# Optimization experiments

Hardware: AMD Instinct MI355X
Metric: run time of the kernel (lower is better)

The kernel has to match this reference:

```python
import jax, jax.numpy as jnp
import numpy as np

B, S, D, U = 8, 2048, 512, 512
L0, L1 = 128, 128  # limit_context (left, right)


def setup_inputs() -> dict:
    key = jax.random.key(0)
    ks = jax.random.split(key, 7)
    scale = 1.0 / np.sqrt(D).astype(np.float32)
    return {
        "x": jax.random.normal(ks[0], (B, S, D), dtype=jnp.float32),
        "Wq": jax.random.normal(ks[1], (D, U), dtype=jnp.float32) * scale,
        "Wk": jax.random.normal(ks[2], (D, U), dtype=jnp.float32) * scale,
        "Wv": jax.random.normal(ks[3], (D, U), dtype=jnp.float32) * scale,
        "bq": jnp.zeros((U,), dtype=jnp.float32),
        "bk": jnp.zeros((U,), dtype=jnp.float32),
        "bv": jnp.zeros((U,), dtype=jnp.float32),
    }


def reference(x, Wq, Wk, Wv, bq, bk, bv):
    # Linear projections for query / key / value (shared input x)
    q = x @ Wq + bq  # [B,S,U]
    k = x @ Wk + bk  # [B,S,U]
    v = x @ Wv + bv  # [B,S,U]

    inv_sqrt_dv = jnp.float32(1.0 / np.sqrt(U))
    scores = jnp.einsum("bqd,bkd->bqk", q, k) * inv_sqrt_dv  # [B,S,S]

    # Sliding-window mask: key j visible to query i iff i-L0 <= j <= i+L1.
    # Equivalent to the original per-step softmax over values[:, start:end].
    i = jnp.arange(S)[:, None]
    j = jnp.arange(S)[None, :]
    window = (j >= i - L0) & (j <= i + L1)  # [S,S]
    neg_inf = jnp.finfo(scores.dtype).min
    scores = jnp.where(window[None], scores, neg_inf)

    attn = jax.nn.softmax(scores, axis=-1)  # [B,S,S]
    return jnp.einsum("bqk,bkd->bqd", attn, v)  # [B,S,U]
```

## Files before the change

kernel.cpp:

```cpp
#include <hip/hip_runtime.h>

#define BATCH 8
#define S_LEN 2048
#define DDIM 512
#define UDIM 512
#define WIN_L 128
#define WIN_R 128
#define PP 296

typedef _Float16 f16;
typedef __attribute__((ext_vector_type(8))) _Float16 f16x8;
typedef __attribute__((ext_vector_type(4))) _Float16 f16x4;
typedef __attribute__((ext_vector_type(4))) float f32x4;

__device__ __forceinline__ void gload_lds16(const void* g, void* l) {
  __builtin_amdgcn_global_load_lds((const __attribute__((address_space(1))) void*)g,
                                   (__attribute__((address_space(3))) void*)l, 16, 0, 0);
}

__global__ void cast_f32_f16(const float* __restrict__ in, f16* __restrict__ out, int n) {
  int i = (blockIdx.x * blockDim.x + threadIdx.x) * 4;
  if (i < n) {
    float4 v = *(const float4*)(in + i);
    f16x4 o;
    o[0] = (f16)v.x; o[1] = (f16)v.y; o[2] = (f16)v.z; o[3] = (f16)v.w;
    *(f16x4*)(out + i) = o;
  }
}

__global__ void transpose_w(const float* __restrict__ Wq, const float* __restrict__ Wk,
                            const float* __restrict__ Wv, f16* __restrict__ WT) {
  const float* W = blockIdx.z == 0 ? Wq : (blockIdx.z == 1 ? Wk : Wv);
  f16* WTz = WT + (size_t)blockIdx.z * DDIM * UDIM;
  __shared__ float t[32][33];
  int tx = threadIdx.x & 31, ty = threadIdx.x >> 5;
  int n0 = blockIdx.x * 32, k0 = blockIdx.y * 32;
  for (int i = 0; i < 4; i++) {
    int r = ty * 4 + i;
    t[r][tx] = W[(size_t)(k0 + r) * UDIM + n0 + tx];
  }
  __syncthreads();
  for (int i = 0; i < 4; i++) {
    int r = ty * 4 + i;
    WTz[(size_t)(n0 + r) * DDIM + k0 + tx] = (f16)t[tx][r];
  }
}

__global__ __launch_bounds__(256, 2) void gemm_qkv(
    const f16* __restrict__ X, const f16* __restrict__ WT,
    const float* __restrict__ bq, const float* __restrict__ bk, const float* __restrict__ bv,
    f16* __restrict__ QKV, f16* __restrict__ VT) {
  int z = blockIdx.z;
  const f16* WTz = WT + (size_t)z * DDIM * UDIM;
  const float* bias = z == 0 ? bq : (z == 1 ? bk : bv);
  f16* out = QKV + (size_t)z * (BATCH * S_LEN) * UDIM;

  __shared__ f16 Al[2][128 * 32];
  __shared__ f16 Bl[2][128 * 32];

  int tid = threadIdx.x, wv = tid >> 6, ln = tid & 63;
  int m0 = blockIdx.x * 128, n0 = blockIdx.y * 128;
  int wm = (wv >> 1) * 64, wn = (wv & 1) * 64;
  int lm = ln & 15, lq = ln >> 4;
  int srow = ln >> 2, scol = (ln & 3) * 8;

  f32x4 acc[4][4];
  for (int mt = 0; mt < 4; mt++)
    for (int nt = 0; nt < 4; nt++)
      for (int r = 0; r < 4; r++) acc[mt][nt][r] = 0.f;

  for (int k0 = 0; k0 < DDIM; k0 += 64) {
    for (int half = 0; half < 2; half++) {
      int r0 = half * 64 + wv * 16;
      for (int c = 0; c < 2; c++) {
        gload_lds16(X + (size_t)(m0 + r0 + srow) * DDIM + k0 + c * 32 + scol, &Al[c][r0 * 32]);
        gload_lds16(WTz + (size_t)(n0 + r0 + srow) * DDIM + k0 + c * 32 + scol, &Bl[c][r0 * 32]);
      }
    }
    __syncthreads();
#pragma unroll
    for (int c = 0; c < 2; c++) {
      f16x8 af[4], bfr[4];
      for (int mt = 0; mt < 4; mt++) af[mt] = *(const f16x8*)&Al[c][(wm + mt * 16 + lm) * 32 + lq * 8];
      for (int nt = 0; nt < 4; nt++) bfr[nt] = *(const f16x8*)&Bl[c][(wn + nt * 16 + lm) * 32 + lq * 8];
      for (int mt = 0; mt < 4; mt++)
        for (int nt = 0; nt < 4; nt++)
          acc[mt][nt] = __builtin_amdgcn_mfma_f32_16x16x32_f16(af[mt], bfr[nt], acc[mt][nt], 0, 0, 0);
    }
    __syncthreads();
  }

  if (z == 2) {
    for (int mt = 0; mt < 4; mt++)
      for (int nt = 0; nt < 4; nt++) {
        int col = n0 + wn + nt * 16 + lm;
        float bv_ = bias[col];
        int row0 = m0 + wm + mt * 16 + lq * 4;
        int bb = row0 >> 11, ss = row0 & 2047;
        f16x4 o;
        for (int r = 0; r < 4; r++) o[r] = (f16)(acc[mt][nt][r] + bv_);
        *(f16x4*)&VT[((size_t)bb * UDIM + col) * S_LEN + ss] = o;
      }
  } else {
    for (int mt = 0; mt < 4; mt++)
      for (int nt = 0; nt < 4; nt++) {
        int col = n0 + wn + nt * 16 + lm;
        float bv_ = bias[col];
        for (int r = 0; r < 4; r++) {
          int row = m0 + wm + mt * 16 + lq * 4 + r;
          out[(size_t)row * UDIM + col] = (f16)(acc[mt][nt][r] + bv_);
        }
      }
  }
}

__global__ __launch_bounds__(256, 2) void attn(
    const f16* __restrict__ Q, const f16* __restrict__ K, const f16* __restrict__ VT,
    float* __restrict__ out) {
  __shared__ f16 Pb[32 * PP];
  __shared__ float wmax[2][32], wsum[2][32];

  int tid = threadIdx.x, wv = tid >> 6, ln = tid & 63;
  int lm = ln & 15, lq = ln >> 4;
  int b = blockIdx.x, q0 = blockIdx.y * 32;
  int rh = wv & 1, ch = wv >> 1;
  const size_t base = (size_t)b * S_LEN;
  const int strip0 = q0 - WIN_L;

  f16x8 qf[16];
  {
    const f16* qrow = Q + (base + q0 + rh * 16 + lm) * (size_t)DDIM + lq * 8;
#pragma unroll
    for (int kk = 0; kk < 16; kk++) qf[kk] = *(const f16x8*)(qrow + kk * 32);
  }

  f32x4 sacc[9];
#pragma unroll
  for (int t = 0; t < 9; t++)
    for (int r = 0; r < 4; r++) sacc[t][r] = 0.f;
#pragma unroll
  for (int t = 0; t < 9; t++) {
    int key = strip0 + ch * 144 + t * 16 + lm;
    int kc = key < 0 ? 0 : (key > S_LEN - 1 ? S_LEN - 1 : key);
    const f16* kp = K + (base + kc) * (size_t)DDIM + lq * 8;
#pragma unroll
    for (int kk = 0; kk < 16; kk++) {
      f16x8 bf = *(const f16x8*)(kp + kk * 32);
      sacc[t] = __builtin_amdgcn_mfma_f32_16x16x32_f16(qf[kk], bf, sacc[t], 0, 0, 0);
    }
  }

  const float scale = 0.044194173824159216f;
  float mx[4] = {-1e30f, -1e30f, -1e30f, -1e30f};
#pragma unroll
  for (int t = 0; t < 9; t++) {
    int kj = strip0 + ch * 144 + t * 16 + lm;
#pragma unroll
    for (int r = 0; r < 4; r++) {
      int qi = q0 + rh * 16 + lq * 4 + r;
      float s = sacc[t][r] * scale;
      bool ok = (kj >= 0) && (kj < S_LEN) && (kj >= qi - WIN_L) && (kj <= qi + WIN_R);
      s = ok ? s : -1e30f;
      sacc[t][r] = s;
      mx[r] = fmaxf(mx[r], s);
    }
  }
#pragma unroll
  for (int r = 0; r < 4; r++) {
    mx[r] = fmaxf(mx[r], __shfl_xor(mx[r], 1));
    mx[r] = fmaxf(mx[r], __shfl_xor(mx[r], 2));
    mx[r] = fmaxf(mx[r], __shfl_xor(mx[r], 4));
    mx[r] = fmaxf(mx[r], __shfl_xor(mx[r], 8));
  }
  if (lm == 0) {
#pragma unroll
    for (int r = 0; r < 4; r++) wmax[ch][rh * 16 + lq * 4 + r] = mx[r];
  }
  __syncthreads();

  float mrow[4], sum[4] = {0.f, 0.f, 0.f, 0.f};
#pragma unroll
  for (int r = 0; r < 4; r++) {
    int row = rh * 16 + lq * 4 + r;
    mrow[r] = fmaxf(wmax[0][row], wmax[1][row]);
  }
#pragma unroll
  for (int t = 0; t < 9; t++) {
#pragma unroll
    for (int r = 0; r < 4; r++) {
      float p = __expf(sacc[t][r] - mrow[r]);
      sum[r] += p;
      Pb[(rh * 16 + lq * 4 + r) * PP + ch * 144 + t * 16 + lm] = (f16)p;
    }
  }
#pragma unroll
  for (int r = 0; r < 4; r++) {
    sum[r] += __shfl_xor(sum[r], 1);
    sum[r] += __shfl_xor(sum[r], 2);
    sum[r] += __shfl_xor(sum[r], 4);
    sum[r] += __shfl_xor(sum[r], 8);
  }
  if (lm == 0) {
#pragma unroll
    for (int r = 0; r < 4; r++) wsum[ch][rh * 16 + lq * 4 + r] = sum[r];
  }
  __syncthreads();

  f32x4 oacc[2][8];
#pragma unroll
  for (int mt = 0; mt < 2; mt++)
    for (int nt = 0; nt < 8; nt++)
      for (int r = 0; r < 4; r++) oacc[mt][nt][r] = 0.f;

  const f16* vbase = VT + ((size_t)b * UDIM + wv * 128 + lm) * S_LEN;
#pragma unroll
  for (int kst = 0; kst < 9; kst++) {
    f16x8 pf0 = *(const f16x8*)&Pb[lm * PP + kst * 32 + lq * 8];
    f16x8 pf1 = *(const f16x8*)&Pb[(16 + lm) * PP + kst * 32 + lq * 8];
    int key = strip0 + kst * 32 + lq * 8;
    int kc = key < 0 ? 0 : (key > S_LEN - 8 ? S_LEN - 8 : key);
#pragma unroll
    for (int nt = 0; nt < 8; nt++) {
      f16x8 vb = *(const f16x8*)(vbase + (size_t)nt * 16 * S_LEN + kc);
      oacc[0][nt] = __builtin_amdgcn_mfma_f32_16x16x32_f16(pf0, vb, oacc[0][nt], 0, 0, 0);
      oacc[1][nt] = __builtin_amdgcn_mfma_f32_16x16x32_f16(pf1, vb, oacc[1][nt], 0, 0, 0);
    }
  }

  float linv[2][4];
#pragma unroll
  for (int mt = 0; mt < 2; mt++)
    for (int r = 0; r < 4; r++) {
      int row = mt * 16 + lq * 4 + r;
      linv[mt][r] = 1.0f / (wsum[0][row] + wsum[1][row]);
    }
#pragma unroll
  for (int mt = 0; mt < 2; mt++)
    for (int nt = 0; nt < 8; nt++)
      for (int r = 0; r < 4; r++) {
        int row = q0 + mt * 16 + lq * 4 + r;
        int col = wv * 128 + nt * 16 + lm;
        out[(base + row) * (size_t)UDIM + col] = oacc[mt][nt][r] * linv[mt][r];
      }
}

extern "C" void kernel_launch(void* const* d_in, const int* in_sizes, int n_in,
                              void* d_out, int out_size, void* d_ws, size_t ws_size,
                              hipStream_t stream) {
  const float* x  = (const float*)d_in[0];
  const float* Wq = (const float*)d_in[1];
  const float* Wk = (const float*)d_in[2];
  const float* Wv = (const float*)d_in[3];
  const float* bq = (const float*)d_in[4];
  const float* bk = (const float*)d_in[5];
  const float* bv = (const float*)d_in[6];
  float* out = (float*)d_out;

  char* ws = (char*)d_ws;
  const size_t XB_BYTES  = (size_t)BATCH * S_LEN * DDIM * 2;
  const size_t WT_BYTES  = (size_t)3 * DDIM * UDIM * 2;
  const size_t QKV_BYTES = (size_t)3 * BATCH * S_LEN * UDIM * 2;
  f16* xb  = (f16*)ws;
  f16* WT  = (f16*)(ws + XB_BYTES);
  f16* QKV = (f16*)(ws + XB_BYTES + WT_BYTES);
  f16* VT  = (f16*)(ws + XB_BYTES + WT_BYTES + QKV_BYTES);

  int n = BATCH * S_LEN * DDIM;
  cast_f32_f16<<<n / (256 * 4), 256, 0, stream>>>(x, xb, n);
  transpose_w<<<dim3(16, 16, 3), 256, 0, stream>>>(Wq, Wk, Wv, WT);
  gemm_qkv<<<dim3(128, 4, 3), 256, 0, stream>>>(xb, WT, bq, bk, bv, QKV, VT);
  attn<<<dim3(BATCH, S_LEN / 32), 256, 0, stream>>>(
      QKV, QKV + (size_t)BATCH * S_LEN * UDIM, VT, out);
}
```

Measured before the change: 182.0 us.

## Shrink attention query tile to 16 rows and stage Q in LDS

The attention kernel now handles 16 query rows per block instead of 32. This doubles the grid and raises the launch-bounds occupancy hint to 4 blocks per CU. Q is loaded into LDS with async global-to-LDS copies, and the 17 key tiles are distributed round-robin across the four waves. Tiles that fall fully outside the sequence skip their MFMAs, and two accumulators interleave the QK products. The trade-off is that each K/V row is now reread by twice as many blocks, so there is less reuse per block.

```diff
diff --git a/kernel.cpp b/kernel.cpp
--- a/kernel.cpp
+++ b/kernel.cpp
@@ -6,7 +6,11 @@
 #define UDIM 512
 #define WIN_L 128
 #define WIN_R 128
+#define QT 16
+#define NSTRIP 272
+#define NTILE 17
 #define PP 296
+#define QP 520
 
 typedef _Float16 f16;
 typedef __attribute__((ext_vector_type(8))) _Float16 f16x8;
@@ -114,54 +118,59 @@
   }
 }
 
-__global__ __launch_bounds__(256, 2) void attn(
+__global__ __launch_bounds__(256, 4) void attn(
     const f16* __restrict__ Q, const f16* __restrict__ K, const f16* __restrict__ VT,
     float* __restrict__ out) {
-  __shared__ f16 Pb[32 * PP];
-  __shared__ float wmax[2][32], wsum[2][32];
+  __shared__ f16 Ql[QT * QP];
+  __shared__ f16 Pb[QT * PP];
+  __shared__ float wmax[4][QT], wsum[4][QT];
 
   int tid = threadIdx.x, wv = tid >> 6, ln = tid & 63;
   int lm = ln & 15, lq = ln >> 4;
-  int b = blockIdx.x, q0 = blockIdx.y * 32;
-  int rh = wv & 1, ch = wv >> 1;
+  int b = blockIdx.x, q0 = blockIdx.y * QT;
   const size_t base = (size_t)b * S_LEN;
   const int strip0 = q0 - WIN_L;
 
-  f16x8 qf[16];
-  {
-    const f16* qrow = Q + (base + q0 + rh * 16 + lm) * (size_t)DDIM + lq * 8;
-#pragma unroll
-    for (int kk = 0; kk < 16; kk++) qf[kk] = *(const f16x8*)(qrow + kk * 32);
-  }
-
-  f32x4 sacc[9];
-#pragma unroll
-  for (int t = 0; t < 9; t++)
-    for (int r = 0; r < 4; r++) sacc[t][r] = 0.f;
-#pragma unroll
-  for (int t = 0; t < 9; t++) {
-    int key = strip0 + ch * 144 + t * 16 + lm;
+  { int zr = tid >> 4, zc = 272 + (tid & 15); Pb[zr * PP + zc] = (f16)0.f; }
+
+  for (int r = 0; r < 4; r++) {
+    int row = wv * 4 + r;
+    gload_lds16(Q + (base + q0 + row) * (size_t)DDIM + ln * 8, &Ql[row * QP]);
+  }
+  __syncthreads();
+
+  const float scale = 0.044194173824159216f;
+  f32x4 sacc[5];
+  float mx[4] = {-1e30f, -1e30f, -1e30f, -1e30f};
+#pragma unroll
+  for (int i = 0; i < 5; i++) {
+    int t = wv + i * 4;
+    if (t >= NTILE) break;
+    int key = strip0 + t * 16 + lm;
+    int t0 = strip0 + t * 16;
+    bool live = (t0 + 15 >= 0) && (t0 < S_LEN);
     int kc = key < 0 ? 0 : (key > S_LEN - 1 ? S_LEN - 1 : key);
     const f16* kp = K + (base + kc) * (size_t)DDIM + lq * 8;
-#pragma unroll
-    for (int kk = 0; kk < 16; kk++) {
-      f16x8 bf = *(const f16x8*)(kp + kk * 32);
-      sacc[t] = __builtin_amdgcn_mfma_f32_16x16x32_f16(qf[kk], bf, sacc[t], 0, 0, 0);
-    }
-  }
-
-  const float scale = 0.044194173824159216f;
-  float mx[4] = {-1e30f, -1e30f, -1e30f, -1e30f};
-#pragma unroll
-  for (int t = 0; t < 9; t++) {
-    int kj = strip0 + ch * 144 + t * 16 + lm;
+    f32x4 s0, s1;
+    for (int r = 0; r < 4; r++) { s0[r] = 0.f; s1[r] = 0.f; }
+    if (live) {
+#pragma unroll
+      for (int kk = 0; kk < 16; kk += 2) {
+        f16x8 qa = *(const f16x8*)&Ql[lm * QP + kk * 32 + lq * 8];
+        f16x8 qb = *(const f16x8*)&Ql[lm * QP + (kk + 1) * 32 + lq * 8];
+        f16x8 k0 = *(const f16x8*)(kp + kk * 32);
+        f16x8 k1 = *(const f16x8*)(kp + (kk + 1) * 32);
+        s0 = __builtin_amdgcn_mfma_f32_16x16x32_f16(qa, k0, s0, 0, 0, 0);
+        s1 = __builtin_amdgcn_mfma_f32_16x16x32_f16(qb, k1, s1, 0, 0, 0);
+      }
+    }
 #pragma unroll
     for (int r = 0; r < 4; r++) {
-      int qi = q0 + rh * 16 + lq * 4 + r;
-      float s = sacc[t][r] * scale;
-      bool ok = (kj >= 0) && (kj < S_LEN) && (kj >= qi - WIN_L) && (kj <= qi + WIN_R);
+      int qi = q0 + lq * 4 + r;
+      float s = (s0[r] + s1[r]) * scale;
+      bool ok = (key >= 0) && (key < S_LEN) && (key >= qi - WIN_L) && (key <= qi + WIN_R);
       s = ok ? s : -1e30f;
-      sacc[t][r] = s;
+      sacc[i][r] = s;
       mx[r] = fmaxf(mx[r], s);
     }
   }
@@ -174,23 +183,25 @@
   }
   if (lm == 0) {
 #pragma unroll
-    for (int r = 0; r < 4; r++) wmax[ch][rh * 16 + lq * 4 + r] = mx[r];
+    for (int r = 0; r < 4; r++) wmax[wv][lq * 4 + r] = mx[r];
   }
   __syncthreads();
 
   float mrow[4], sum[4] = {0.f, 0.f, 0.f, 0.f};
 #pragma unroll
   for (int r = 0; r < 4; r++) {
-    int row = rh * 16 + lq * 4 + r;
-    mrow[r] = fmaxf(wmax[0][row], wmax[1][row]);
-  }
-#pragma unroll
-  for (int t = 0; t < 9; t++) {
+    int row = lq * 4 + r;
+    mrow[r] = fmaxf(fmaxf(wmax[0][row], wmax[1][row]), fmaxf(wmax[2][row], wmax[3][row]));
+  }
+#pragma unroll
+  for (int i = 0; i < 5; i++) {
+    int t = wv + i * 4;
+    if (t >= NTILE) break;
 #pragma unroll
     for (int r = 0; r < 4; r++) {
-      float p = __expf(sacc[t][r] - mrow[r]);
+      float p = __expf(sacc[i][r] - mrow[r]);
       sum[r] += p;
-      Pb[(rh * 16 + lq * 4 + r) * PP + ch * 144 + t * 16 + lm] = (f16)p;
+      Pb[(lq * 4 + r) * PP + t * 16 + lm] = (f16)p;
     }
   }
 #pragma unroll
@@ -202,46 +213,41 @@
   }
   if (lm == 0) {
 #pragma unroll
-    for (int r = 0; r < 4; r++) wsum[ch][rh * 16 + lq * 4 + r] = sum[r];
-  }
-  __syncthreads();
-
-  f32x4 oacc[2][8];
-#pragma unroll
-  for (int mt = 0; mt < 2; mt++)
-    for (int nt = 0; nt < 8; nt++)
-      for (int r = 0; r < 4; r++) oacc[mt][nt][r] = 0.f;
-
-  const f16* vbase = VT + ((size_t)b * UDIM + wv * 128 + lm) * S_LEN;
+    for (int r = 0; r < 4; r++) wsum[wv][lq * 4 + r] = sum[r];
+  }
+  __syncthreads();
+
+  f32x4 oacc[8];
+#pragma unroll
+  for (int nt = 0; nt < 8; nt++)
+    for (int r = 0; r < 4; r++) oacc[nt][r] = 0.f;
+
+  const f16* vb = VT + ((size_t)b * UDIM + wv * 128 + lm) * S_LEN;
 #pragma unroll
   for (int kst = 0; kst < 9; kst++) {
-    f16x8 pf0 = *(const f16x8*)&Pb[lm * PP + kst * 32 + lq * 8];
-    f16x8 pf1 = *(const f16x8*)&Pb[(16 + lm) * PP + kst * 32 + lq * 8];
+    f16x8 pf = *(const f16x8*)&Pb[lm * PP + kst * 32 + lq * 8];
     int key = strip0 + kst * 32 + lq * 8;
     int kc = key < 0 ? 0 : (key > S_LEN - 8 ? S_LEN - 8 : key);
 #pragma unroll
     for (int nt = 0; nt < 8; nt++) {
-      f16x8 vb = *(const f16x8*)(vbase + (size_t)nt * 16 * S_LEN + kc);
-      oacc[0][nt] = __builtin_amdgcn_mfma_f32_16x16x32_f16(pf0, vb, oacc[0][nt], 0, 0, 0);
-      oacc[1][nt] = __builtin_amdgcn_mfma_f32_16x16x32_f16(pf1, vb, oacc[1][nt], 0, 0, 0);
-    }
-  }
-
-  float linv[2][4];
-#pragma unroll
-  for (int mt = 0; mt < 2; mt++)
+      f16x8 vv = *(const f16x8*)(vb + (size_t)(nt * 16) * S_LEN + kc);
+      oacc[nt] = __builtin_amdgcn_mfma_f32_16x16x32_f16(pf, vv, oacc[nt], 0, 0, 0);
+    }
+  }
+
+  float linv[4];
+#pragma unroll
+  for (int r = 0; r < 4; r++) {
+    int row = lq * 4 + r;
+    linv[r] = 1.0f / (wsum[0][row] + wsum[1][row] + wsum[2][row] + wsum[3][row]);
+  }
+#pragma unroll
+  for (int nt = 0; nt < 8; nt++)
     for (int r = 0; r < 4; r++) {
-      int row = mt * 16 + lq * 4 + r;
-      linv[mt][r] = 1.0f / (wsum[0][row] + wsum[1][row]);
-    }
-#pragma unroll
-  for (int mt = 0; mt < 2; mt++)
-    for (int nt = 0; nt < 8; nt++)
-      for (int r = 0; r < 4; r++) {
-        int row = q0 + mt * 16 + lq * 4 + r;
-        int col = wv * 128 + nt * 16 + lm;
-        out[(base + row) * (size_t)UDIM + col] = oacc[mt][nt][r] * linv[mt][r];
-      }
+      int row = q0 + lq * 4 + r;
+      int col = wv * 128 + nt * 16 + lm;
+      out[(base + row) * (size_t)UDIM + col] = oacc[nt][r] * linv[r];
+    }
 }
 
 extern "C" void kernel_launch(void* const* d_in, const int* in_sizes, int n_in,
@@ -269,6 +275,6 @@
   cast_f32_f16<<<n / (256 * 4), 256, 0, stream>>>(x, xb, n);
   transpose_w<<<dim3(16, 16, 3), 256, 0, stream>>>(Wq, Wk, Wv, WT);
   gemm_qkv<<<dim3(128, 4, 3), 256, 0, stream>>>(xb, WT, bq, bk, bv, QKV, VT);
-  attn<<<dim3(BATCH, S_LEN / 32), 256, 0, stream>>>(
+  attn<<<dim3(BATCH, S_LEN / QT), 256, 0, stream>>>(
       QKV, QKV + (size_t)BATCH * S_LEN * UDIM, VT, out);
 }
```

New measurement: 196.4 us. 7.9% more time.

## Stage K and V tiles through shared LDS buffer in windowed attention

Applied to the files above, without the earlier changes.

The QK^T stage now loads each 32-key K tile into LDS once per block with global_load_lds, and every wave reads its MFMA operands from there. Before, each pair of waves re-read the same K rows straight from global memory. The PV stage likewise loads 32-key V^T tiles cooperatively into a padded LDS buffer that reuses the same memory. Wave roles are remapped to row-half by key-half, and tiles that fall fully outside the sequence are skipped. In exchange it adds two block barriers per tile step and more LDS use, which may reduce latency hiding between waves.

```diff
diff --git a/kernel.cpp b/kernel.cpp
--- a/kernel.cpp
+++ b/kernel.cpp
@@ -6,6 +6,8 @@
 #define UDIM 512
 #define WIN_L 128
 #define WIN_R 128
+#define KP 520
+#define VP 40
 #define PP 296
 
 typedef _Float16 f16;
@@ -117,13 +119,16 @@
 __global__ __launch_bounds__(256, 2) void attn(
     const f16* __restrict__ Q, const f16* __restrict__ K, const f16* __restrict__ VT,
     float* __restrict__ out) {
+  __shared__ __align__(16) char ubuf[VP * 512 * 2];
   __shared__ f16 Pb[32 * PP];
   __shared__ float wmax[2][32], wsum[2][32];
+  f16* Kl = (f16*)ubuf;
+  f16* Vl = (f16*)ubuf;
 
   int tid = threadIdx.x, wv = tid >> 6, ln = tid & 63;
   int lm = ln & 15, lq = ln >> 4;
   int b = blockIdx.x, q0 = blockIdx.y * 32;
-  int rh = wv & 1, ch = wv >> 1;
+  int rh = wv >> 1, kh = wv & 1;
   const size_t base = (size_t)b * S_LEN;
   const int strip0 = q0 - WIN_L;
 
@@ -136,33 +141,48 @@
 
   f32x4 sacc[9];
 #pragma unroll
-  for (int t = 0; t < 9; t++)
-    for (int r = 0; r < 4; r++) sacc[t][r] = 0.f;
-#pragma unroll
-  for (int t = 0; t < 9; t++) {
-    int key = strip0 + ch * 144 + t * 16 + lm;
-    int kc = key < 0 ? 0 : (key > S_LEN - 1 ? S_LEN - 1 : key);
-    const f16* kp = K + (base + kc) * (size_t)DDIM + lq * 8;
-#pragma unroll
-    for (int kk = 0; kk < 16; kk++) {
-      f16x8 bf = *(const f16x8*)(kp + kk * 32);
-      sacc[t] = __builtin_amdgcn_mfma_f32_16x16x32_f16(qf[kk], bf, sacc[t], 0, 0, 0);
+  for (int s = 0; s < 9; s++)
+    for (int r = 0; r < 4; r++) sacc[s][r] = 0.f;
+
+#pragma unroll
+  for (int s = 0; s < 9; s++) {
+    int j0 = strip0 + s * 32;
+    if (j0 + 31 >= 0 && j0 < S_LEN) {
+#pragma unroll
+      for (int i = 0; i < 8; i++) {
+        int row = wv * 8 + i;
+        int key = j0 + row;
+        int kc = key < 0 ? 0 : (key > S_LEN - 1 ? S_LEN - 1 : key);
+        gload_lds16(K + (base + kc) * (size_t)DDIM + ln * 8, &Kl[row * KP]);
+      }
+      __syncthreads();
+      f32x4 s0, s1;
+      for (int r = 0; r < 4; r++) { s0[r] = 0.f; s1[r] = 0.f; }
+#pragma unroll
+      for (int kk = 0; kk < 16; kk += 2) {
+        f16x8 b0 = *(const f16x8*)&Kl[(kh * 16 + lm) * KP + kk * 32 + lq * 8];
+        f16x8 b1 = *(const f16x8*)&Kl[(kh * 16 + lm) * KP + (kk + 1) * 32 + lq * 8];
+        s0 = __builtin_amdgcn_mfma_f32_16x16x32_f16(qf[kk], b0, s0, 0, 0, 0);
+        s1 = __builtin_amdgcn_mfma_f32_16x16x32_f16(qf[kk + 1], b1, s1, 0, 0, 0);
+      }
+      for (int r = 0; r < 4; r++) sacc[s][r] = s0[r] + s1[r];
+      __syncthreads();
     }
   }
 
   const float scale = 0.044194173824159216f;
   float mx[4] = {-1e30f, -1e30f, -1e30f, -1e30f};
 #pragma unroll
-  for (int t = 0; t < 9; t++) {
-    int kj = strip0 + ch * 144 + t * 16 + lm;
+  for (int s = 0; s < 9; s++) {
+    int kj = strip0 + s * 32 + kh * 16 + lm;
 #pragma unroll
     for (int r = 0; r < 4; r++) {
       int qi = q0 + rh * 16 + lq * 4 + r;
-      float s = sacc[t][r] * scale;
+      float v = sacc[s][r] * scale;
       bool ok = (kj >= 0) && (kj < S_LEN) && (kj >= qi - WIN_L) && (kj <= qi + WIN_R);
-      s = ok ? s : -1e30f;
-      sacc[t][r] = s;
-      mx[r] = fmaxf(mx[r], s);
+      v = ok ? v : -1e30f;
+      sacc[s][r] = v;
+      mx[r] = fmaxf(mx[r], v);
     }
   }
 #pragma unroll
@@ -174,7 +194,7 @@
   }
   if (lm == 0) {
 #pragma unroll
-    for (int r = 0; r < 4; r++) wmax[ch][rh * 16 + lq * 4 + r] = mx[r];
+    for (int r = 0; r < 4; r++) wmax[kh][rh * 16 + lq * 4 + r] = mx[r];
   }
   __syncthreads();
 
@@ -185,12 +205,12 @@
     mrow[r] = fmaxf(wmax[0][row], wmax[1][row]);
   }
 #pragma unroll
-  for (int t = 0; t < 9; t++) {
+  for (int s = 0; s < 9; s++) {
 #pragma unroll
     for (int r = 0; r < 4; r++) {
-      float p = __expf(sacc[t][r] - mrow[r]);
+      float p = __expf(sacc[s][r] - mrow[r]);
       sum[r] += p;
-      Pb[(rh * 16 + lq * 4 + r) * PP + ch * 144 + t * 16 + lm] = (f16)p;
+      Pb[(rh * 16 + lq * 4 + r) * PP + s * 32 + kh * 16 + lm] = (f16)p;
     }
   }
 #pragma unroll
@@ -202,7 +222,7 @@
   }
   if (lm == 0) {
 #pragma unroll
-    for (int r = 0; r < 4; r++) wsum[ch][rh * 16 + lq * 4 + r] = sum[r];
+    for (int r = 0; r < 4; r++) wsum[kh][rh * 16 + lq * 4 + r] = sum[r];
   }
   __syncthreads();
 
@@ -212,19 +232,28 @@
     for (int nt = 0; nt < 8; nt++)
       for (int r = 0; r < 4; r++) oacc[mt][nt][r] = 0.f;
 
-  const f16* vbase = VT + ((size_t)b * UDIM + wv * 128 + lm) * S_LEN;
-#pragma unroll
-  for (int kst = 0; kst < 9; kst++) {
-    f16x8 pf0 = *(const f16x8*)&Pb[lm * PP + kst * 32 + lq * 8];
-    f16x8 pf1 = *(const f16x8*)&Pb[(16 + lm) * PP + kst * 32 + lq * 8];
-    int key = strip0 + kst * 32 + lq * 8;
-    int kc = key < 0 ? 0 : (key > S_LEN - 8 ? S_LEN - 8 : key);
+  for (int t = 0; t < 9; t++) {
+    int j0 = strip0 + t * 32;
+    if (j0 + 31 < 0 || j0 >= S_LEN) continue;
+#pragma unroll
+    for (int i = 0; i < 8; i++) {
+      int u = i * 64 + (tid >> 2);
+      int c4 = tid & 3;
+      int key = j0 + c4 * 8;
+      int kc = key < 0 ? 0 : (key > S_LEN - 8 ? S_LEN - 8 : key);
+      f16x8 v = *(const f16x8*)(VT + ((size_t)b * UDIM + u) * S_LEN + kc);
+      *(f16x8*)&Vl[u * VP + c4 * 8] = v;
+    }
+    __syncthreads();
+    f16x8 pf0 = *(const f16x8*)&Pb[lm * PP + t * 32 + lq * 8];
+    f16x8 pf1 = *(const f16x8*)&Pb[(16 + lm) * PP + t * 32 + lq * 8];
 #pragma unroll
     for (int nt = 0; nt < 8; nt++) {
-      f16x8 vb = *(const f16x8*)(vbase + (size_t)nt * 16 * S_LEN + kc);
-      oacc[0][nt] = __builtin_amdgcn_mfma_f32_16x16x32_f16(pf0, vb, oacc[0][nt], 0, 0, 0);
-      oacc[1][nt] = __builtin_amdgcn_mfma_f32_16x16x32_f16(pf1, vb, oacc[1][nt], 0, 0, 0);
-    }
+      f16x8 vv = *(const f16x8*)&Vl[(wv * 128 + nt * 16 + lm) * VP + lq * 8];
+      oacc[0][nt] = __builtin_amdgcn_mfma_f32_16x16x32_f16(pf0, vv, oacc[0][nt], 0, 0, 0);
+      oacc[1][nt] = __builtin_amdgcn_mfma_f32_16x16x32_f16(pf1, vv, oacc[1][nt], 0, 0, 0);
+    }
+    __syncthreads();
   }
 
   float linv[2][4];
```

After: 155.0 us. -14.8%, faster.
